# Performance work log

Hardware: AMD Instinct MI355X
Metric: run time of the kernel (lower is better)

## Reference

```python
import jax, jax.numpy as jnp
import numpy as np

CHUNK_SIZE = 2048
EPS = 1e-12  # torch F.normalize clamps the norm at 1e-12


def _l2_normalize(x, axis):
    n = jnp.sqrt(jnp.sum(x * x, axis=axis, keepdims=True))
    return x / jnp.maximum(n, EPS)


def _nnfm_loss(F_r, F_s, chunk_size=CHUNK_SIZE):
    B, C, H_r, W_r = F_r.shape
    _, _, H_s, W_s = F_s.shape
    N_r = H_r * W_r
    N_s = H_s * W_s
    assert N_r % chunk_size == 0, "N_r must be divisible by chunk_size for this reference"
    n_chunks = N_r // chunk_size

    F_s_norm = _l2_normalize(F_s.reshape(B, C, N_s), axis=1)  # (B, C, N_s)
    F_r_flat = F_r.reshape(B, C, N_r)
    # (n_chunks, B, C, chunk) -- contiguous chunks along N_r, matching the torch loop
    chunks = F_r_flat.reshape(B, C, n_chunks, chunk_size).transpose(2, 0, 1, 3)

    def body(chunk):  # chunk: (B, C, chunk_size)
        cn = _l2_normalize(chunk, axis=1)
        sim = jnp.einsum('bcn,bcm->bnm', cn, F_s_norm)  # (B, chunk, N_s)
        # min(1 - sim) over N_s == 1 - max(sim)
        return 1.0 - jnp.max(sim, axis=2)  # (B, chunk)

    min_dists = jax.lax.map(body, chunks)  # (n_chunks, B, chunk) -- bounded memory
    return jnp.mean(min_dists)


def setup_inputs() -> dict:
    key = jax.random.key(0)
    k1, k2 = jax.random.split(key)
    F_r = jax.random.normal(k1, (1, 768, 128, 128), dtype=jnp.float32)
    F_s = jax.random.normal(k2, (1, 768, 128, 128), dtype=jnp.float32)
    return {"F_r": F_r, "F_s": F_s}


def reference(F_r, F_s):
    return _nnfm_loss(F_r, F_s)
```

## Files before the change

kernel.cpp:

```cpp
#include <hip/hip_runtime.h>
#include <cstdint>
#include <cstddef>

#define C_DIM 768
#define N_DIM 16384

typedef __attribute__((ext_vector_type(8))) short short8;
typedef __attribute__((ext_vector_type(4))) float f32x4;

__device__ __forceinline__ ushort f2bf(float f) {
    uint32_t u = __float_as_uint(f);
    uint32_t r = 0x7fffu + ((u >> 16) & 1u);
    return (ushort)((u + r) >> 16);
}

__device__ __forceinline__ void async_ld16(const void* g, void* l) {
    __builtin_amdgcn_global_load_lds(
        (__attribute__((address_space(1))) void*)g,
        (__attribute__((address_space(3))) void*)l,
        16, 0, 0);
}

__global__ __launch_bounds__(256) void norm_tr(const float* __restrict__ F0,
                                               ushort* __restrict__ T0,
                                               const float* __restrict__ F1,
                                               ushort* __restrict__ T1) {
    const float*  F = blockIdx.y ? F1 : F0;
    ushort*       T = blockIdx.y ? T1 : T0;
    const int i0 = blockIdx.x * 64;
    const int t  = threadIdx.x;
    const int tx = t & 63;
    const int ty = t >> 6;

    float ss = 0.f;
    for (int c = ty; c < C_DIM; c += 4) {
        float v = F[(size_t)c * N_DIM + i0 + tx];
        ss += v * v;
    }
    __shared__ float red[4][64];
    __shared__ float scale[64];
    red[ty][tx] = ss;
    __syncthreads();
    if (t < 64) {
        float s = red[0][t] + red[1][t] + red[2][t] + red[3][t];
        float n = sqrtf(s);
        scale[t] = 1.0f / fmaxf(n, 1e-12f);
    }
    __syncthreads();

    __shared__ float tile[64][65];
    const int i_l   = t >> 3;
    const int c_off = (t & 7) * 8;
    for (int c0 = 0; c0 < C_DIM; c0 += 64) {
        #pragma unroll
        for (int rr = 0; rr < 16; ++rr) {
            int c_l = rr * 4 + ty;
            tile[c_l][tx] = F[(size_t)(c0 + c_l) * N_DIM + i0 + tx] * scale[tx];
        }
        __syncthreads();
        #pragma unroll
        for (int half = 0; half < 2; ++half) {
            int il = i_l + half * 32;
            __align__(16) ushort pack[8];
            #pragma unroll
            for (int j = 0; j < 8; ++j)
                pack[j] = f2bf(tile[c_off + j][il]);
            *(uint4*)&T[(size_t)(i0 + il) * C_DIM + c0 + c_off] = *(const uint4*)pack;
        }
        __syncthreads();
    }
}

__global__ __launch_bounds__(256) void gemm_rowmax(const ushort* __restrict__ A,
                                                   const ushort* __restrict__ B,
                                                   unsigned* __restrict__ rowkey) {
    __shared__ __align__(16) ushort As[2][128 * 32];
    __shared__ __align__(16) ushort Bs[2][128 * 32];

    const int t    = threadIdx.x;
    const int lane = t & 63;
    const int w    = t >> 6;
    const int wm   = w >> 1, wn = w & 1;

    const int bid   = blockIdx.x;
    const int xcd   = bid & 7;
    const int local = bid >> 3;
    const int half_ = local >> 10;
    const int rem   = local & 1023;
    const int m0    = (rem >> 3) * 128;
    const int n0    = (xcd * 16 + half_ * 8 + (rem & 7)) * 128;

    f32x4 acc[4][4];
    #pragma unroll
    for (int i = 0; i < 4; ++i)
        #pragma unroll
        for (int j = 0; j < 4; ++j)
            acc[i][j] = (f32x4){0.f, 0.f, 0.f, 0.f};

    const int r  = t >> 2;
    const int kq = ((t & 3) ^ ((t >> 3) & 3)) * 8;
    const ushort* ag0 = A + (size_t)(m0 + r) * C_DIM + kq;
    const ushort* ag1 = ag0 + (size_t)64 * C_DIM;
    const ushort* bg0 = B + (size_t)(n0 + r) * C_DIM + kq;
    const ushort* bg1 = bg0 + (size_t)64 * C_DIM;
    const int ld0 = t * 8, ld1 = 64 * 32 + t * 8;

    const int qp    = ((lane >> 4) ^ ((lane >> 1) & 3)) * 8;
    const int a_off = (wm * 64 + (lane & 15)) * 32 + qp;
    const int b_off = (wn * 64 + (lane & 15)) * 32 + qp;

    async_ld16(ag0, As[0] + ld0);
    async_ld16(ag1, As[0] + ld1);
    async_ld16(bg0, Bs[0] + ld0);
    async_ld16(bg1, Bs[0] + ld1);

    int buf = 0;
    for (int k0 = 0; k0 < C_DIM; k0 += 32) {
        __syncthreads();
        if (k0 + 32 < C_DIM) {
            const int kn = k0 + 32, nb = buf ^ 1;
            async_ld16(ag0 + kn, As[nb] + ld0);
            async_ld16(ag1 + kn, As[nb] + ld1);
            async_ld16(bg0 + kn, Bs[nb] + ld0);
            async_ld16(bg1 + kn, Bs[nb] + ld1);
        }

        const ushort* Ab = As[buf];
        const ushort* Bb = Bs[buf];
        short8 af[4], bfr[4];
        #pragma unroll
        for (int mt = 0; mt < 4; ++mt)
            af[mt] = *(const short8*)(Ab + a_off + mt * 16 * 32);
        #pragma unroll
        for (int nt = 0; nt < 4; ++nt)
            bfr[nt] = *(const short8*)(Bb + b_off + nt * 16 * 32);
        #pragma unroll
        for (int mt = 0; mt < 4; ++mt)
            #pragma unroll
            for (int nt = 0; nt < 4; ++nt)
                acc[mt][nt] = __builtin_amdgcn_mfma_f32_16x16x32_bf16(
                    af[mt], bfr[nt], acc[mt][nt], 0, 0, 0);
        buf ^= 1;
    }

    #pragma unroll
    for (int mt = 0; mt < 4; ++mt) {
        #pragma unroll
        for (int reg = 0; reg < 4; ++reg) {
            float v = fmaxf(fmaxf(acc[mt][0][reg], acc[mt][1][reg]),
                            fmaxf(acc[mt][2][reg], acc[mt][3][reg]));
            #pragma unroll
            for (int off = 1; off < 16; off <<= 1)
                v = fmaxf(v, __shfl_xor(v, off, 64));
            if ((lane & 15) == 0) {
                int m = m0 + wm * 64 + mt * 16 + (lane >> 4) * 4 + reg;
                unsigned u = __float_as_uint(v);
                u = (u & 0x80000000u) ? ~u : (u | 0x80000000u);
                atomicMax(&rowkey[m], u);
            }
        }
    }
}

__global__ __launch_bounds__(1024) void finalize(const unsigned* __restrict__ rowkey,
                                                 float* __restrict__ out) {
    const int t = threadIdx.x;
    float s = 0.f;
    for (int i = t; i < N_DIM; i += 1024) {
        unsigned u = rowkey[i];
        float f = (u & 0x80000000u) ? __uint_as_float(u ^ 0x80000000u)
                                    : __uint_as_float(~u);
        s += f;
    }
    #pragma unroll
    for (int off = 32; off >= 1; off >>= 1)
        s += __shfl_down(s, off, 64);
    __shared__ float part[16];
    if ((t & 63) == 0) part[t >> 6] = s;
    __syncthreads();
    if (t == 0) {
        float tot = 0.f;
        #pragma unroll
        for (int i = 0; i < 16; ++i) tot += part[i];
        out[0] = 1.0f - tot * (1.0f / (float)N_DIM);
    }
}

extern "C" void kernel_launch(void* const* d_in, const int* in_sizes, int n_in,
                              void* d_out, int out_size, void* d_ws, size_t ws_size,
                              hipStream_t stream) {
    const float* F_r = (const float*)d_in[0];
    const float* F_s = (const float*)d_in[1];

    ushort*   Rt     = (ushort*)d_ws;
    ushort*   St     = Rt + (size_t)N_DIM * C_DIM;
    unsigned* rowkey = (unsigned*)(St + (size_t)N_DIM * C_DIM);
    float*    out    = (float*)d_out;

    hipLaunchKernelGGL(norm_tr, dim3(N_DIM / 64, 2), dim3(256), 0, stream,
                       F_r, Rt, F_s, St);
    hipMemsetAsync(rowkey, 0, N_DIM * sizeof(unsigned), stream);
    hipLaunchKernelGGL(gemm_rowmax, dim3(N_DIM / 128 * N_DIM / 128), dim3(256),
                       0, stream, Rt, St, rowkey);
    hipLaunchKernelGGL(finalize, dim3(1), dim3(1024), 0, stream, rowkey, out);
}
```

Before: 692.9 us.

## Widen GEMM block tile to 128x256 with 8 waves per block

The bf16 similarity GEMM now uses 512-thread blocks covering a 128x256 output tile (2x4 waves, 64x64 each) instead of 128x128 with 4 waves. Each loaded A tile is reused across twice as many columns, which cuts global/L2 traffic per FLOP and halves the number of blocks and row-max atomics. The XCD-aware block mapping is rewritten for the new grid. In exchange LDS use per block grows, which may lower occupancy, and larger blocks synchronize more waves at each barrier.

```diff
diff --git a/kernel.cpp b/kernel.cpp
--- a/kernel.cpp
+++ b/kernel.cpp
@@ -71,24 +71,23 @@
     }
 }
 
-__global__ __launch_bounds__(256) void gemm_rowmax(const ushort* __restrict__ A,
+__global__ __launch_bounds__(512) void gemm_rowmax(const ushort* __restrict__ A,
                                                    const ushort* __restrict__ B,
                                                    unsigned* __restrict__ rowkey) {
     __shared__ __align__(16) ushort As[2][128 * 32];
-    __shared__ __align__(16) ushort Bs[2][128 * 32];
+    __shared__ __align__(16) ushort Bs[2][256 * 32];
 
     const int t    = threadIdx.x;
     const int lane = t & 63;
     const int w    = t >> 6;
-    const int wm   = w >> 1, wn = w & 1;
+    const int wm   = w >> 2;
+    const int wn   = w & 3;
 
     const int bid   = blockIdx.x;
     const int xcd   = bid & 7;
     const int local = bid >> 3;
-    const int half_ = local >> 10;
-    const int rem   = local & 1023;
-    const int m0    = (rem >> 3) * 128;
-    const int n0    = (xcd * 16 + half_ * 8 + (rem & 7)) * 128;
+    const int m0    = (local >> 3) * 128;
+    const int n0    = (xcd * 8 + (local & 7)) * 256;
 
     f32x4 acc[4][4];
     #pragma unroll
@@ -97,32 +96,29 @@
         for (int j = 0; j < 4; ++j)
             acc[i][j] = (f32x4){0.f, 0.f, 0.f, 0.f};
 
-    const int r  = t >> 2;
     const int kq = ((t & 3) ^ ((t >> 3) & 3)) * 8;
-    const ushort* ag0 = A + (size_t)(m0 + r) * C_DIM + kq;
-    const ushort* ag1 = ag0 + (size_t)64 * C_DIM;
-    const ushort* bg0 = B + (size_t)(n0 + r) * C_DIM + kq;
-    const ushort* bg1 = bg0 + (size_t)64 * C_DIM;
-    const int ld0 = t * 8, ld1 = 64 * 32 + t * 8;
+    const ushort* ag  = A + (size_t)(m0 + (t >> 2)) * C_DIM + kq;
+    const ushort* bg0 = B + (size_t)(n0 + (t >> 2)) * C_DIM + kq;
+    const ushort* bg1 = bg0 + (size_t)128 * C_DIM;
+    const int lda = t * 8;
+    const int ldb0 = t * 8, ldb1 = 128 * 32 + t * 8;
 
     const int qp    = ((lane >> 4) ^ ((lane >> 1) & 3)) * 8;
     const int a_off = (wm * 64 + (lane & 15)) * 32 + qp;
     const int b_off = (wn * 64 + (lane & 15)) * 32 + qp;
 
-    async_ld16(ag0, As[0] + ld0);
-    async_ld16(ag1, As[0] + ld1);
-    async_ld16(bg0, Bs[0] + ld0);
-    async_ld16(bg1, Bs[0] + ld1);
+    async_ld16(ag,  As[0] + lda);
+    async_ld16(bg0, Bs[0] + ldb0);
+    async_ld16(bg1, Bs[0] + ldb1);
 
     int buf = 0;
     for (int k0 = 0; k0 < C_DIM; k0 += 32) {
         __syncthreads();
         if (k0 + 32 < C_DIM) {
             const int kn = k0 + 32, nb = buf ^ 1;
-            async_ld16(ag0 + kn, As[nb] + ld0);
-            async_ld16(ag1 + kn, As[nb] + ld1);
-            async_ld16(bg0 + kn, Bs[nb] + ld0);
-            async_ld16(bg1 + kn, Bs[nb] + ld1);
+            async_ld16(ag + kn,  As[nb] + lda);
+            async_ld16(bg0 + kn, Bs[nb] + ldb0);
+            async_ld16(bg1 + kn, Bs[nb] + ldb1);
         }
 
         const ushort* Ab = As[buf];
@@ -200,7 +196,7 @@
     hipLaunchKernelGGL(norm_tr, dim3(N_DIM / 64, 2), dim3(256), 0, stream,
                        F_r, Rt, F_s, St);
     hipMemsetAsync(rowkey, 0, N_DIM * sizeof(unsigned), stream);
-    hipLaunchKernelGGL(gemm_rowmax, dim3(N_DIM / 128 * N_DIM / 128), dim3(256),
+    hipLaunchKernelGGL(gemm_rowmax, dim3((N_DIM / 128) * (N_DIM / 256)), dim3(512),
                        0, stream, Rt, St, rowkey);
     hipLaunchKernelGGL(finalize, dim3(1), dim3(1024), 0, stream, rowkey, out);
 }
```

New measurement: 692.0 us. Within noise of the previous version (-0.1%).
